# Performance work log

Measured on AMD Instinct MI355X. Metric: run time of the kernel, lower is better.

## Reference

```python
import jax, jax.numpy as jnp
import numpy as np

T, B, N, L = 4, 8, 25000, 64
D_IN = 1 + 2 * L  # node_dim + latent + time_dim


def setup_inputs() -> dict:
    key = jax.random.key(0)
    ks = jax.random.split(key, 20)
    f = lambda k, shp, s=0.1: jax.random.normal(k, shp, dtype=jnp.float32) * s
    z = lambda shp: jnp.zeros(shp, jnp.float32)
    return dict(
        raw=f(ks[0], (T, B, N, 1), 1.0),
        r_label=f(ks[1], (T, B, N, 1), 1.0),
        t=jax.random.uniform(ks[2], (T, B, N, 1), dtype=jnp.float32) * 100.0,
        src=jax.random.randint(ks[3], (T, B), 0, N, dtype=jnp.int32),
        tar=jax.random.randint(ks[4], (T, B), 0, N, dtype=jnp.int32),
        n_mask=jax.random.randint(ks[5], (T, B, N), 0, 2, dtype=jnp.int32),
        w_t=f(ks[6], (L,)), b_t=f(ks[7], (L,)),
        W_msg=f(ks[8], (1 + L, L)), b_msg=z((L,)),
        Wi=f(ks[9], (L, 3 * L)), Wh=f(ks[10], (L, 3 * L)),
        bi=z((3 * L,)), bh=z((3 * L,)),
        Wq=f(ks[11], (D_IN, L)), bq=z((L,)),
        Wk=f(ks[12], (D_IN, L)), bk=z((L,)),
        Wv=f(ks[13], (D_IN, L)), bv=z((L,)),
        W_out=f(ks[14], (L, 1)), b_out=z((1,)),
    )


def reference(raw, r_label, t, src, tar, n_mask, w_t, b_t, W_msg, b_msg,
              Wi, Wh, bi, bh, Wq, bq, Wk, bk, Wv, bv, W_out, b_out):
    Ldim = w_t.shape[0]
    Bdim, Ndim = raw.shape[1], raw.shape[2]
    bidx = jnp.arange(Bdim)
    scale = 1.0 / jnp.sqrt(jnp.float32(Ldim))
    enc0 = jnp.cos(b_t)  # time encoding of t=0 for the target query

    def time_enc(tt):  # [..., 1] -> [..., L]
        return jnp.cos(tt * w_t + b_t)

    def gru(x, h):  # torch.nn.GRUCell math
        gi = x @ Wi + bi
        gh = h @ Wh + bh
        ir, iz, inn = jnp.split(gi, 3, axis=-1)
        hr, hz, hn = jnp.split(gh, 3, axis=-1)
        rg = jax.nn.sigmoid(ir + hr)
        zg = jax.nn.sigmoid(iz + hz)
        ng = jnp.tanh(inn + rg * hn)
        return (1.0 - zg) * ng + zg * h

    def step(carry, inp):
        memory, r = carry            # [N,L], [B,N,1]
        t_b, tar_b, mask_b, rlab_b = inp  # [B,N,1], [B], [B,N], [N,1]
        enc_t = time_enc(t_b)        # [B,N,L]
        # 1. memory update (message from last batch element, GRU over all nodes)
        msg = jnp.concatenate([r[-1], enc_t[-1]], axis=-1) @ W_msg + b_msg  # [N,L]
        mem2 = gru(msg, memory)      # [N,L]
        # 2. embedding: target query over all node features
        tar_r = r[bidx, tar_b]       # [B,1]
        tar_hid = mem2[tar_b]        # [B,L]
        tar_h = jnp.concatenate(
            [tar_r, tar_hid, jnp.broadcast_to(enc0, (Bdim, Ldim))], axis=-1)  # [B,1+2L]
        h = jnp.concatenate(
            [r, jnp.broadcast_to(mem2[None], (Bdim, Ndim, Ldim)), enc_t], axis=-1)  # [B,N,1+2L]
        q = tar_h @ Wq + bq          # [B,L]
        k = h @ Wk + bk              # [B,N,L]
        v = h @ Wv + bv              # [B,N,L]
        scores = jnp.einsum('bl,bnl->bn', q, k) * scale
        scores = jnp.where(mask_b > 0, scores, jnp.float32(-1e9))
        attn = jax.nn.softmax(scores, axis=-1)
        z = jnp.einsum('bn,bnl->bl', attn, v)  # [B,L]
        logit = z @ W_out + b_out    # [B,1]
        # vectorized scatter replacing the python loop r_pred[tar_id]=pred_logit
        r_pred = r[-1].at[tar_b].set(logit)    # [N,1]
        r_last = 0.5 * (r_pred + rlab_b)       # teacher forcing blend
        r_next = jnp.broadcast_to(r_last[None], (Bdim, Ndim, 1))
        return (mem2, r_next), logit

    mem0 = jnp.zeros((Ndim, Ldim), jnp.float32)
    rlab_last = r_label[:, -1]  # [T,N,1]
    (_, _), logits = jax.lax.scan(step, (mem0, raw[0]), (t, tar, n_mask, rlab_last))
    return logits  # [T,B,1]
```

## Files before the change

kernel.cpp:

```cpp
#include <hip/hip_runtime.h>
#include <math.h>

#define TSTEPS 4
#define BB 8
#define NN 25000
#define LLD 64
#define DIN 129

#define OFF_W6    0
#define OFF_I4    24576
#define OFF_R4    24832
#define OFF_A     25088
#define OFF_WQ0   33473
#define OFF_CA    33602
#define OFF_C0Q   33667
#define OFF_WVO   33668
#define OFF_C0    33797
#define OFF_U     33798
#define OFF_BFRAG 36864
#define OFF_MEMA  73728
#define OFF_MEMB  1673728
#define OFF_RLAST 3273728
#define OFF_PART  3298728
#define NBLK 98
#define PSTRIDE 132

typedef short s16x8 __attribute__((ext_vector_type(8)));
typedef float f32x4 __attribute__((ext_vector_type(4)));

__device__ __forceinline__ float sigm(float x) { return 1.f / (1.f + __expf(-x)); }
__device__ __forceinline__ float tanh_fast(float x) {
  float ax = fabsf(x);
  float e = __expf(-2.f * ax);
  float t = (1.f - e) / (1.f + e);
  return copysignf(t, x);
}
__device__ __forceinline__ float wred_max(float v) {
#pragma unroll
  for (int m = 32; m; m >>= 1) v = fmaxf(v, __shfl_xor(v, m));
  return v;
}
__device__ __forceinline__ float wred_sum(float v) {
#pragma unroll
  for (int m = 32; m; m >>= 1) v += __shfl_xor(v, m);
  return v;
}
__device__ __forceinline__ unsigned short bf16_rne(float v) {
  unsigned int u = __float_as_uint(v);
  unsigned int r = (u + 0x7FFFu + ((u >> 16) & 1u)) >> 16;
  return (unsigned short)r;
}
__device__ __forceinline__ float bf16_to_f(unsigned short b) {
  return __uint_as_float(((unsigned int)b) << 16);
}

__global__ __launch_bounds__(64) void k_setup_u(
    const float* __restrict__ Wq, const float* __restrict__ bq,
    const float* __restrict__ b_t, float* __restrict__ ws) {
  int j = threadIdx.x;
  float acc = bq[j];
  for (int l = 0; l < 64; l++) acc += __cosf(b_t[l]) * Wq[(65 + l) * 64 + j];
  ws[OFF_U + j] = acc;
}

__global__ __launch_bounds__(1024) void k_setup(
    const float* __restrict__ W_msg, const float* __restrict__ Wi,
    const float* __restrict__ bi, const float* __restrict__ b_msg,
    const float* __restrict__ bh, const float* __restrict__ Wh,
    const float* __restrict__ Wq, const float* __restrict__ bq,
    const float* __restrict__ Wk, const float* __restrict__ bk,
    const float* __restrict__ Wv, const float* __restrict__ bv,
    const float* __restrict__ W_out, const float* __restrict__ b_out,
    const float* __restrict__ b_t, float* __restrict__ ws) {
  int id = blockIdx.x * 1024 + threadIdx.x;
  if (id < 24576) {
    int k = id / 384, rem = id % 384, l = rem / 6, g = rem % 6;
    float acc = 0.f;
    if (g < 3) {
      for (int m = 0; m < 64; m++) acc += W_msg[(k + 1) * 64 + m] * Wi[m * 192 + g * 64 + l];
    } else {
      acc = Wh[k * 192 + (g - 3) * 64 + l];
    }
    ws[OFF_W6 + id] = acc;
  } else if (id < 24832) {
    int id2 = id - 24576, l = id2 / 4, g = id2 % 4;
    float v;
    if (g == 3) v = bh[128 + l];
    else {
      int j = g * 64 + l;
      float bcf = bi[j];
      for (int m = 0; m < 64; m++) bcf += b_msg[m] * Wi[m * 192 + j];
      v = (g < 2) ? (bcf + bh[j]) : bcf;
    }
    ws[OFF_I4 + id2] = v;
  } else if (id < 25088) {
    int id2 = id - 24832, l = id2 / 4, g = id2 % 4;
    float v = 0.f;
    if (g < 3) {
      for (int m = 0; m < 64; m++) v += W_msg[m] * Wi[m * 192 + g * 64 + l];
    }
    ws[OFF_R4 + id2] = v;
  } else if (id < 33473) {
    int id3 = id - 25088, d = id3 / 65, i = id3 % 65;
    float acc = 0.f;
    for (int j = 0; j < 64; j++) acc += Wk[d * 64 + j] * Wq[i * 64 + j];
    ws[OFF_A + id3] = acc;
  } else if (id < 33602) {
    int d = id - 33473;
    float acc = 0.f;
    for (int j = 0; j < 64; j++) acc += Wk[d * 64 + j] * ws[OFF_U + j];
    ws[OFF_WQ0 + d] = acc;
  } else if (id < 33667) {
    int i = id - 33602;
    float acc = 0.f;
    for (int j = 0; j < 64; j++) acc += bk[j] * Wq[i * 64 + j];
    ws[OFF_CA + i] = acc;
  } else if (id == 33667) {
    float acc = 0.f;
    for (int j = 0; j < 64; j++) acc += bk[j] * ws[OFF_U + j];
    ws[OFF_C0Q] = acc;
  } else if (id < 33797) {
    int d = id - 33668;
    float acc = 0.f;
    for (int j = 0; j < 64; j++) acc += Wv[d * 64 + j] * W_out[j];
    ws[OFF_WVO + d] = acc;
  } else if (id == 33797) {
    float acc = b_out[0];
    for (int j = 0; j < 64; j++) acc += bv[j] * W_out[j];
    ws[OFF_C0] = acc;
  }
}

__global__ __launch_bounds__(1024) void k_pack(
    const float* __restrict__ ws_r, float* __restrict__ ws) {
  int id = blockIdx.x * 1024 + threadIdx.x;
  int r = id & 7, lane = (id >> 3) & 63, kt = (id >> 9) & 3, ct = id >> 11;
  int col = 16 * ct + (lane & 15);
  int k = 32 * kt + ((lane >> 4) << 3) + r;
  int a = col >> 6, l = col & 63;
  float w = 0.f;
  if (k < 64) {
    if (a < 3) w = ws_r[OFF_W6 + (k * 64 + l) * 6 + a];
  } else {
    int k2 = k - 64;
    if (a == 0) w = ws_r[OFF_W6 + (k2 * 64 + l) * 6 + 3];
    else if (a == 1) w = ws_r[OFF_W6 + (k2 * 64 + l) * 6 + 4];
    else if (a == 3) w = ws_r[OFF_W6 + (k2 * 64 + l) * 6 + 5];
  }
  unsigned short hb = bf16_rne(w);
  unsigned short lb = bf16_rne(w - bf16_to_f(hb));
  unsigned short* BFu = (unsigned short*)(ws + OFF_BFRAG);
  int idx = ((ct * 4 + kt) * 64 + lane) * 8 + r;
  BFu[idx] = hb;
  BFu[32768 + idx] = lb;
}

__global__ __launch_bounds__(256, 2) void k_gru(
    const float* __restrict__ t_in, const float* __restrict__ raw,
    const float* __restrict__ r_last, const float* __restrict__ w_t,
    const float* __restrict__ b_t, const float* __restrict__ i4p,
    const float* __restrict__ r4p, const unsigned short* __restrict__ BF,
    const float* __restrict__ memPrev, float* __restrict__ memNext, int tt) {
  __shared__ unsigned short XhiS[64 * 136];
  __shared__ unsigned short XloS[64 * 136];
  __shared__ float out_lds[64 * 65];
  __shared__ float tb_lds[64], rn_lds[64];
  int tid = threadIdx.x;
  int lane = tid & 63;
  int wv = tid >> 6;
  int nbase = blockIdx.x * 64;

  if (tid < 64) {
    int nc = min(nbase + tid, NN - 1);
    tb_lds[tid] = t_in[(tt * BB + BB - 1) * NN + nc];
    rn_lds[tid] = (tt == 0) ? raw[(BB - 1) * NN + nc] : r_last[nc];
  }
  __syncthreads();

  {
    int nl = lane;
    int nc = min(nbase + nl, NN - 1);
    float tb = tb_lds[nl];
    int swz = (nl & 7) << 3;
#pragma unroll
    for (int c = 0; c < 4; c++) {
      int kc = wv * 32 + c * 8;
      s16x8 h8, l8;
#pragma unroll
      for (int j = 0; j < 8; j++) {
        int k = kc + j;
        float v;
        if (k < 64) v = __cosf(tb * w_t[k] + b_t[k]);
        else v = (tt == 0) ? 0.f : memPrev[(k - 64) * NN + nc];
        unsigned short hb = bf16_rne(v);
        unsigned short lb = bf16_rne(v - bf16_to_f(hb));
        h8[j] = (short)hb;
        l8[j] = (short)lb;
      }
      int off = nl * 136 + (kc ^ swz);
      *(s16x8*)(XhiS + off) = h8;
      *(s16x8*)(XloS + off) = l8;
    }
  }
  __syncthreads();

  const s16x8* BF8 = (const s16x8*)BF;
  f32x4 acc[4][4];
#pragma unroll
  for (int g = 0; g < 4; g++)
#pragma unroll
    for (int m = 0; m < 4; m++) acc[g][m] = (f32x4){0.f, 0.f, 0.f, 0.f};

  int swzA = (lane & 7) << 3;
#pragma unroll
  for (int kt = 0; kt < 4; kt++) {
    s16x8 bh[4], bl[4];
#pragma unroll
    for (int g = 0; g < 4; g++) {
      int ct = wv + 4 * g;
      bh[g] = BF8[(ct * 4 + kt) * 64 + lane];
      bl[g] = BF8[4096 + (ct * 4 + kt) * 64 + lane];
    }
#pragma unroll
    for (int m = 0; m < 4; m++) {
      int row = 16 * m + (lane & 15);
      int off = row * 136 + ((32 * kt + 8 * (lane >> 4)) ^ swzA);
      s16x8 ah = *(const s16x8*)(XhiS + off);
      s16x8 al = *(const s16x8*)(XloS + off);
#pragma unroll
      for (int g = 0; g < 4; g++) {
        acc[g][m] = __builtin_amdgcn_mfma_f32_16x16x32_bf16(ah, bh[g], acc[g][m], 0, 0, 0);
        acc[g][m] = __builtin_amdgcn_mfma_f32_16x16x32_bf16(ah, bl[g], acc[g][m], 0, 0, 0);
        acc[g][m] = __builtin_amdgcn_mfma_f32_16x16x32_bf16(al, bh[g], acc[g][m], 0, 0, 0);
      }
    }
  }

  int myl = 16 * wv + (lane & 15);
  float4 iv = ((const float4*)i4p)[myl];
  float4 rv = ((const float4*)r4p)[myl];
  int kmem = 64 + myl;
  int slot = kmem & ~7;
  int wel = kmem & 7;
#pragma unroll
  for (int m = 0; m < 4; m++) {
#pragma unroll
    for (int i = 0; i < 4; i++) {
      int nloc = 16 * m + (lane >> 4) * 4 + i;
      float rn = rn_lds[nloc];
      float gRv = acc[0][m][i] + iv.x + rn * rv.x;
      float gZv = acc[1][m][i] + iv.y + rn * rv.y;
      float aNv = acc[2][m][i] + iv.z + rn * rv.z;
      float hNv = acc[3][m][i] + iv.w;
      float rg = sigm(gRv);
      float zg = sigm(gZv);
      float ng = tanh_fast(aNv + rg * hNv);
      int offm = nloc * 136 + (slot ^ ((nloc & 7) << 3)) + wel;
      float mp = bf16_to_f(XhiS[offm]) + bf16_to_f(XloS[offm]);
      out_lds[myl * 65 + nloc] = (1.f - zg) * ng + zg * mp;
    }
  }
  __syncthreads();
#pragma unroll
  for (int jj = 0; jj < 16; jj++) {
    int l2 = jj * 4 + wv;
    int n = nbase + lane;
    if (n < NN) memNext[l2 * NN + n] = out_lds[l2 * 65 + lane];
  }
}

__global__ __launch_bounds__(256) void k_attn(
    const float* __restrict__ t_in, const float* __restrict__ raw,
    const float* __restrict__ r_last, const int* __restrict__ n_mask,
    const float* __restrict__ w_t, const float* __restrict__ b_t,
    const int* __restrict__ tar, const float* __restrict__ A,
    const float* __restrict__ wq0, const float* __restrict__ cA,
    const float* __restrict__ c0q, const float* __restrict__ mem2,
    float* __restrict__ part, int tt) {
  __shared__ float m2t[64];
  __shared__ float wq_lds[132];
  __shared__ float e_sh[256], t_sh[256];
  __shared__ float red4[4], redS[4], redR[4];
  __shared__ float pm[2][64], pe[2][64];

  int tid = threadIdx.x;
  int lane = tid & 63;
  int wvid = tid >> 6;
  int b = blockIdx.y;
  int n0 = blockIdx.x * 256;
  int n = n0 + tid;
  int nc = min(n, NN - 1);
  bool valid = (n < NN);
  int tarn = tar[tt * BB + b];

  if (tid < 64) m2t[tid] = mem2[tid * NN + tarn];
  __syncthreads();
  float tr = (tt == 0) ? raw[b * NN + tarn] : r_last[tarn];
  if (tid < 129) {
    const float* Ar = A + tid * 65;
    float acc = wq0[tid] + tr * Ar[0];
#pragma unroll 8
    for (int k = 0; k < 64; k++) acc += m2t[k] * Ar[1 + k];
    wq_lds[tid] = acc;
  } else if (tid == 129) {
    float acc = c0q[0] + tr * cA[0];
    for (int k = 0; k < 64; k++) acc += m2t[k] * cA[1 + k];
    wq_lds[129] = acc;
  }

  float tb = t_in[(tt * BB + b) * NN + nc];
  int mk = n_mask[(tt * BB + b) * NN + nc];
  float rn = (tt == 0) ? raw[b * NN + nc] : r_last[nc];
  __syncthreads();

  float sc = rn * wq_lds[0];
#pragma unroll 8
  for (int d = 0; d < 64; d++) sc += mem2[d * NN + nc] * wq_lds[1 + d];
#pragma unroll 8
  for (int l = 0; l < 64; l++) sc += __cosf(tb * w_t[l] + b_t[l]) * wq_lds[65 + l];
  float score = (sc + wq_lds[129]) * 0.125f;
  bool act = valid && (mk > 0);

  float mw = wred_max(act ? score : -1e30f);
  if (lane == 0) red4[wvid] = mw;
  __syncthreads();
  float mb = fmaxf(fmaxf(red4[0], red4[1]), fmaxf(red4[2], red4[3]));

  float e = act ? __expf(score - mb) : 0.f;
  float sw = wred_sum(e);
  float sr = wred_sum(e * rn);
  if (lane == 0) { redS[wvid] = sw; redR[wvid] = sr; }
  e_sh[tid] = e;
  t_sh[tid] = tb;
  __syncthreads();
  float Sb = redS[0] + redS[1] + redS[2] + redS[3];
  float Rb = redR[0] + redR[1] + redR[2] + redR[3];

  if (wvid < 2) {
    const float* mrow = mem2 + lane * NN + n0;
    int i0 = wvid * 128;
    float acc = 0.f;
#pragma unroll 4
    for (int i = i0; i < i0 + 128; i++) acc += e_sh[i] * mrow[i];
    pm[wvid][lane] = acc;
  } else {
    float wl = w_t[lane], bl = b_t[lane];
    int i0 = (wvid - 2) * 128;
    float acc = 0.f;
#pragma unroll 4
    for (int i = i0; i < i0 + 128; i++) acc += e_sh[i] * __cosf(t_sh[i] * wl + bl);
    pe[wvid - 2][lane] = acc;
  }
  __syncthreads();

  int pbase = (b * NBLK + blockIdx.x) * PSTRIDE;
  if (tid < 64) part[pbase + 1 + tid] = pm[0][tid] + pm[1][tid];
  else if (tid < 128) part[pbase + 65 + (tid - 64)] = pe[0][tid - 64] + pe[1][tid - 64];
  else if (tid == 128) part[pbase + 0] = Rb;
  else if (tid == 129) part[pbase + 129] = mb;
  else if (tid == 130) part[pbase + 130] = Sb;
}

__global__ __launch_bounds__(256) void k_merge(
    const float* __restrict__ part, const float* __restrict__ wvo,
    const float* __restrict__ c0p, const int* __restrict__ tar,
    const float* __restrict__ raw, const float* __restrict__ r_label,
    float* __restrict__ r_last, float* __restrict__ out, int tt) {
  int tid = threadIdx.x;
  if (blockIdx.x < NBLK) {
    int n = blockIdx.x * 256 + tid;
    if (n >= NN) return;
    bool istar = false;
#pragma unroll
    for (int b = 0; b < BB; b++) istar |= (tar[tt * BB + b] == n);
    if (istar) return;
    float base = (tt == 0) ? raw[(BB - 1) * NN + n] : r_last[n];
    r_last[n] = 0.5f * (base + r_label[(tt * BB + BB - 1) * NN + n]);
    return;
  }

  int b = blockIdx.x - NBLK;
  const float* pb = part + b * NBLK * PSTRIDE;
  __shared__ float red[256], fac[NBLK];

  red[tid] = (tid < NBLK) ? pb[tid * PSTRIDE + 129] : -1e30f;
  __syncthreads();
  for (int s = 128; s > 0; s >>= 1) {
    if (tid < s) red[tid] = fmaxf(red[tid], red[tid + s]);
    __syncthreads();
  }
  float mb = red[0];
  __syncthreads();
  if (tid < NBLK) fac[tid] = __expf(pb[tid * PSTRIDE + 129] - mb);
  __syncthreads();
  red[tid] = (tid < NBLK) ? pb[tid * PSTRIDE + 130] * fac[tid] : 0.f;
  __syncthreads();
  for (int s = 128; s > 0; s >>= 1) {
    if (tid < s) red[tid] += red[tid + s];
    __syncthreads();
  }
  float Sb = red[0];
  __syncthreads();

  float acc = 0.f;
  if (tid < DIN) {
    for (int j = 0; j < NBLK; j++) acc += fac[j] * pb[j * PSTRIDE + tid];
    acc *= wvo[tid];
  }
  red[tid] = (tid < DIN) ? acc : 0.f;
  __syncthreads();
  for (int s = 128; s > 0; s >>= 1) {
    if (tid < s) red[tid] += red[tid + s];
    __syncthreads();
  }
  if (tid == 0) {
    float lg = red[0] / Sb + c0p[0];
    out[tt * BB + b] = lg;
    int mytar = tar[tt * BB + b];
    bool last = true;
    for (int bb = b + 1; bb < BB; bb++)
      if (tar[tt * BB + bb] == mytar) last = false;
    if (last)
      r_last[mytar] = 0.5f * (lg + r_label[(tt * BB + BB - 1) * NN + mytar]);
  }
}

extern "C" void kernel_launch(void* const* d_in, const int* in_sizes, int n_in,
                              void* d_out, int out_size, void* d_ws, size_t ws_size,
                              hipStream_t stream) {
  const float* raw     = (const float*)d_in[0];
  const float* r_label = (const float*)d_in[1];
  const float* t_in    = (const float*)d_in[2];
  const int*   tar     = (const int*)d_in[4];
  const int*   n_mask  = (const int*)d_in[5];
  const float* w_t     = (const float*)d_in[6];
  const float* b_t     = (const float*)d_in[7];
  const float* W_msg   = (const float*)d_in[8];
  const float* b_msg   = (const float*)d_in[9];
  const float* Wi      = (const float*)d_in[10];
  const float* Wh      = (const float*)d_in[11];
  const float* bi      = (const float*)d_in[12];
  const float* bh      = (const float*)d_in[13];
  const float* Wq      = (const float*)d_in[14];
  const float* bq      = (const float*)d_in[15];
  const float* Wk      = (const float*)d_in[16];
  const float* bk      = (const float*)d_in[17];
  const float* Wv      = (const float*)d_in[18];
  const float* bv      = (const float*)d_in[19];
  const float* W_out   = (const float*)d_in[20];
  const float* b_out   = (const float*)d_in[21];

  float* ws  = (float*)d_ws;
  float* out = (float*)d_out;

  k_setup_u<<<1, 64, 0, stream>>>(Wq, bq, b_t, ws);
  k_setup<<<34, 1024, 0, stream>>>(W_msg, Wi, bi, b_msg, bh, Wh, Wq, bq, Wk, bk,
                                   Wv, bv, W_out, b_out, b_t, ws);
  k_pack<<<32, 1024, 0, stream>>>(ws, ws);

  for (int tt = 0; tt < TSTEPS; tt++) {
    float* mp = ws + ((tt & 1) ? OFF_MEMB : OFF_MEMA);
    float* mn = ws + ((tt & 1) ? OFF_MEMA : OFF_MEMB);
    k_gru<<<dim3((NN + 63) / 64), dim3(256), 0, stream>>>(
        t_in, raw, ws + OFF_RLAST, w_t, b_t,
        ws + OFF_I4, ws + OFF_R4, (const unsigned short*)(ws + OFF_BFRAG),
        mp, mn, tt);
    k_attn<<<dim3(NBLK, BB), dim3(256), 0, stream>>>(
        t_in, raw, ws + OFF_RLAST, n_mask, w_t, b_t, tar,
        ws + OFF_A, ws + OFF_WQ0, ws + OFF_CA, ws + OFF_C0Q,
        mn, ws + OFF_PART, tt);
    k_merge<<<dim3(NBLK + BB), dim3(256), 0, stream>>>(
        ws + OFF_PART, ws + OFF_WVO, ws + OFF_C0, tar,
        raw, r_label, ws + OFF_RLAST, out, tt);
  }
}
```

Baseline: 211.5 us.

## Switch GRU memory to node-major layout and fold setup_u into setup

```diff
diff --git a/kernel.cpp b/kernel.cpp
--- a/kernel.cpp
+++ b/kernel.cpp
@@ -16,7 +16,6 @@
 #define OFF_C0Q   33667
 #define OFF_WVO   33668
 #define OFF_C0    33797
-#define OFF_U     33798
 #define OFF_BFRAG 36864
 #define OFF_MEMA  73728
 #define OFF_MEMB  1673728
@@ -52,15 +51,6 @@
 }
 __device__ __forceinline__ float bf16_to_f(unsigned short b) {
   return __uint_as_float(((unsigned int)b) << 16);
-}
-
-__global__ __launch_bounds__(64) void k_setup_u(
-    const float* __restrict__ Wq, const float* __restrict__ bq,
-    const float* __restrict__ b_t, float* __restrict__ ws) {
-  int j = threadIdx.x;
-  float acc = bq[j];
-  for (int l = 0; l < 64; l++) acc += __cosf(b_t[l]) * Wq[(65 + l) * 64 + j];
-  ws[OFF_U + j] = acc;
 }
 
 __global__ __launch_bounds__(1024) void k_setup(
@@ -72,7 +62,27 @@
     const float* __restrict__ Wv, const float* __restrict__ bv,
     const float* __restrict__ W_out, const float* __restrict__ b_out,
     const float* __restrict__ b_t, float* __restrict__ ws) {
-  int id = blockIdx.x * 1024 + threadIdx.x;
+  if (blockIdx.x == 0) {
+    __shared__ float u_lds[64];
+    int tid = threadIdx.x;
+    if (tid < 64) {
+      float acc = bq[tid];
+      for (int l = 0; l < 64; l++) acc += __cosf(b_t[l]) * Wq[(65 + l) * 64 + tid];
+      u_lds[tid] = acc;
+    }
+    __syncthreads();
+    if (tid < 129) {
+      float acc = 0.f;
+      for (int j = 0; j < 64; j++) acc += Wk[tid * 64 + j] * u_lds[j];
+      ws[OFF_WQ0 + tid] = acc;
+    } else if (tid == 129) {
+      float acc = 0.f;
+      for (int j = 0; j < 64; j++) acc += bk[j] * u_lds[j];
+      ws[OFF_C0Q] = acc;
+    }
+    return;
+  }
+  int id = (blockIdx.x - 1) * 1024 + threadIdx.x;
   if (id < 24576) {
     int k = id / 384, rem = id % 384, l = rem / 6, g = rem % 6;
     float acc = 0.f;
@@ -105,26 +115,17 @@
     float acc = 0.f;
     for (int j = 0; j < 64; j++) acc += Wk[d * 64 + j] * Wq[i * 64 + j];
     ws[OFF_A + id3] = acc;
-  } else if (id < 33602) {
-    int d = id - 33473;
-    float acc = 0.f;
-    for (int j = 0; j < 64; j++) acc += Wk[d * 64 + j] * ws[OFF_U + j];
-    ws[OFF_WQ0 + d] = acc;
-  } else if (id < 33667) {
-    int i = id - 33602;
+  } else if (id < 33538) {
+    int i = id - 33473;
     float acc = 0.f;
     for (int j = 0; j < 64; j++) acc += bk[j] * Wq[i * 64 + j];
     ws[OFF_CA + i] = acc;
-  } else if (id == 33667) {
-    float acc = 0.f;
-    for (int j = 0; j < 64; j++) acc += bk[j] * ws[OFF_U + j];
-    ws[OFF_C0Q] = acc;
-  } else if (id < 33797) {
-    int d = id - 33668;
+  } else if (id < 33667) {
+    int d = id - 33538;
     float acc = 0.f;
     for (int j = 0; j < 64; j++) acc += Wv[d * 64 + j] * W_out[j];
     ws[OFF_WVO + d] = acc;
-  } else if (id == 33797) {
+  } else if (id == 33667) {
     float acc = b_out[0];
     for (int j = 0; j < 64; j++) acc += bv[j] * W_out[j];
     ws[OFF_C0] = acc;
@@ -157,13 +158,12 @@
 
 __global__ __launch_bounds__(256, 2) void k_gru(
     const float* __restrict__ t_in, const float* __restrict__ raw,
-    const float* __restrict__ r_last, const float* __restrict__ w_t,
+    const float* __restrict__ r_in, const float* __restrict__ w_t,
     const float* __restrict__ b_t, const float* __restrict__ i4p,
     const float* __restrict__ r4p, const unsigned short* __restrict__ BF,
     const float* __restrict__ memPrev, float* __restrict__ memNext, int tt) {
   __shared__ unsigned short XhiS[64 * 136];
   __shared__ unsigned short XloS[64 * 136];
-  __shared__ float out_lds[64 * 65];
   __shared__ float tb_lds[64], rn_lds[64];
   int tid = threadIdx.x;
   int lane = tid & 63;
@@ -173,7 +173,7 @@
   if (tid < 64) {
     int nc = min(nbase + tid, NN - 1);
     tb_lds[tid] = t_in[(tt * BB + BB - 1) * NN + nc];
-    rn_lds[tid] = (tt == 0) ? raw[(BB - 1) * NN + nc] : r_last[nc];
+    rn_lds[tid] = (tt == 0) ? raw[(BB - 1) * NN + nc] : r_in[nc];
   }
   __syncthreads();
 
@@ -182,20 +182,30 @@
     int nc = min(nbase + nl, NN - 1);
     float tb = tb_lds[nl];
     int swz = (nl & 7) << 3;
+    const float4* mp4 = (const float4*)(memPrev + (size_t)nc * 64);
 #pragma unroll
     for (int c = 0; c < 4; c++) {
       int kc = wv * 32 + c * 8;
+      float vv[8];
+      if (kc < 64) {
+#pragma unroll
+        for (int j = 0; j < 8; j++) vv[j] = __cosf(tb * w_t[kc + j] + b_t[kc + j]);
+      } else if (tt == 0) {
+#pragma unroll
+        for (int j = 0; j < 8; j++) vv[j] = 0.f;
+      } else {
+        int d0 = kc - 64;
+        float4 f0 = mp4[d0 >> 2];
+        float4 f1 = mp4[(d0 >> 2) + 1];
+        vv[0] = f0.x; vv[1] = f0.y; vv[2] = f0.z; vv[3] = f0.w;
+        vv[4] = f1.x; vv[5] = f1.y; vv[6] = f1.z; vv[7] = f1.w;
+      }
       s16x8 h8, l8;
 #pragma unroll
       for (int j = 0; j < 8; j++) {
-        int k = kc + j;
-        float v;
-        if (k < 64) v = __cosf(tb * w_t[k] + b_t[k]);
-        else v = (tt == 0) ? 0.f : memPrev[(k - 64) * NN + nc];
-        unsigned short hb = bf16_rne(v);
-        unsigned short lb = bf16_rne(v - bf16_to_f(hb));
+        unsigned short hb = bf16_rne(vv[j]);
         h8[j] = (short)hb;
-        l8[j] = (short)lb;
+        l8[j] = (short)bf16_rne(vv[j] - bf16_to_f(hb));
       }
       int off = nl * 136 + (kc ^ swz);
       *(s16x8*)(XhiS + off) = h8;
@@ -257,15 +267,9 @@
       float ng = tanh_fast(aNv + rg * hNv);
       int offm = nloc * 136 + (slot ^ ((nloc & 7) << 3)) + wel;
       float mp = bf16_to_f(XhiS[offm]) + bf16_to_f(XloS[offm]);
-      out_lds[myl * 65 + nloc] = (1.f - zg) * ng + zg * mp;
-    }
-  }
-  __syncthreads();
-#pragma unroll
-  for (int jj = 0; jj < 16; jj++) {
-    int l2 = jj * 4 + wv;
-    int n = nbase + lane;
-    if (n < NN) memNext[l2 * NN + n] = out_lds[l2 * 65 + lane];
+      int n = nbase + nloc;
+      if (n < NN) memNext[(size_t)n * 64 + myl] = (1.f - zg) * ng + zg * mp;
+    }
   }
 }
 
@@ -293,7 +297,7 @@
   bool valid = (n < NN);
   int tarn = tar[tt * BB + b];
 
-  if (tid < 64) m2t[tid] = mem2[tid * NN + tarn];
+  if (tid < 64) m2t[tid] = mem2[(size_t)tarn * 64 + tid];
   __syncthreads();
   float tr = (tt == 0) ? raw[b * NN + tarn] : r_last[tarn];
   if (tid < 129) {
@@ -314,8 +318,13 @@
   __syncthreads();
 
   float sc = rn * wq_lds[0];
-#pragma unroll 8
-  for (int d = 0; d < 64; d++) sc += mem2[d * NN + nc] * wq_lds[1 + d];
+  const float4* m4 = (const float4*)(mem2 + (size_t)nc * 64);
+#pragma unroll
+  for (int q = 0; q < 16; q++) {
+    float4 v = m4[q];
+    sc += v.x * wq_lds[1 + 4 * q] + v.y * wq_lds[2 + 4 * q] +
+          v.z * wq_lds[3 + 4 * q] + v.w * wq_lds[4 + 4 * q];
+  }
 #pragma unroll 8
   for (int l = 0; l < 64; l++) sc += __cosf(tb * w_t[l] + b_t[l]) * wq_lds[65 + l];
   float score = (sc + wq_lds[129]) * 0.125f;
@@ -337,11 +346,13 @@
   float Rb = redR[0] + redR[1] + redR[2] + redR[3];
 
   if (wvid < 2) {
-    const float* mrow = mem2 + lane * NN + n0;
     int i0 = wvid * 128;
     float acc = 0.f;
 #pragma unroll 4
-    for (int i = i0; i < i0 + 128; i++) acc += e_sh[i] * mrow[i];
+    for (int i = i0; i < i0 + 128; i++) {
+      int ii = min(n0 + i, NN - 1);
+      acc += e_sh[i] * mem2[(size_t)ii * 64 + lane];
+    }
     pm[wvid][lane] = acc;
   } else {
     float wl = w_t[lane], bl = b_t[lane];
@@ -404,8 +415,16 @@
 
   float acc = 0.f;
   if (tid < DIN) {
-    for (int j = 0; j < NBLK; j++) acc += fac[j] * pb[j * PSTRIDE + tid];
-    acc *= wvo[tid];
+    float a0 = 0.f, a1 = 0.f, a2 = 0.f, a3 = 0.f;
+    int j = 0;
+    for (; j + 3 < NBLK; j += 4) {
+      a0 += fac[j] * pb[j * PSTRIDE + tid];
+      a1 += fac[j + 1] * pb[(j + 1) * PSTRIDE + tid];
+      a2 += fac[j + 2] * pb[(j + 2) * PSTRIDE + tid];
+      a3 += fac[j + 3] * pb[(j + 3) * PSTRIDE + tid];
+    }
+    for (; j < NBLK; j++) a0 += fac[j] * pb[j * PSTRIDE + tid];
+    acc = ((a0 + a1) + (a2 + a3)) * wvo[tid];
   }
   red[tid] = (tid < DIN) ? acc : 0.f;
   __syncthreads();
@@ -453,7 +472,6 @@
   float* ws  = (float*)d_ws;
   float* out = (float*)d_out;
 
-  k_setup_u<<<1, 64, 0, stream>>>(Wq, bq, b_t, ws);
   k_setup<<<34, 1024, 0, stream>>>(W_msg, Wi, bi, b_msg, bh, Wh, Wq, bq, Wk, bk,
                                    Wv, bv, W_out, b_out, b_t, ws);
   k_pack<<<32, 1024, 0, stream>>>(ws, ws);
```

Result: faster. 194.9 us (-7.8%).
